# Optimization experiments

Measured on AMD Instinct MI355X. Metric: run time of the kernel, lower is better.

Reference implementation:

```python
import jax, jax.numpy as jnp
import numpy as np

N_NODES = 50000
N_EDGES = 640000
IN_C, HID_C, OUT_C = 64, 128, 64


def _glorot(key, fan_in, fan_out):
    lim = float(np.sqrt(6.0 / (fan_in + fan_out)))
    return jax.random.uniform(key, (fan_in, fan_out), jnp.float32, -lim, lim)


def setup_inputs() -> dict:
    key = jax.random.key(0)
    ks = jax.random.split(key, 16)
    x = jax.random.normal(ks[0], (N_NODES, IN_C), jnp.float32)
    edge_index = jax.random.randint(ks[1], (2, N_EDGES), 0, N_NODES, jnp.int64)
    # SAGEConv params: out = mean_aggr(x_j) @ Wl + x @ Wr + b
    dims = [(IN_C, HID_C), (HID_C, HID_C), (HID_C, OUT_C)]
    params = {}
    for i, (fi, fo) in enumerate(dims):
        params[f"Wl{i}"] = _glorot(ks[2 + 3 * i], fi, fo)
        params[f"Wr{i}"] = _glorot(ks[3 + 3 * i], fi, fo)
        params[f"b{i}"] = jnp.zeros((fo,), jnp.float32)
    # classifier: Linear(64,32) -> ReLU -> Linear(32,1) -> Sigmoid (dropout off in eval)
    params["Wc1"] = _glorot(ks[11], OUT_C, 32)
    params["bc1"] = jnp.zeros((32,), jnp.float32)
    params["Wc2"] = _glorot(ks[12], 32, 1)
    params["bc2"] = jnp.zeros((1,), jnp.float32)
    return {"x": x, "edge_index": edge_index, **params}


def _sage_conv(x, src, dst, Wl, Wr, b):
    # gather neighbor (source) features along edges, mean-aggregate at target
    msgs = x[src]                                                    # [E, C]
    agg = jax.ops.segment_sum(msgs, dst, num_segments=N_NODES)      # [N, C]
    deg = jax.ops.segment_sum(jnp.ones((src.shape[0], 1), x.dtype), dst,
                              num_segments=N_NODES)                 # [N, 1]
    agg = agg / jnp.maximum(deg, 1.0)
    return agg @ Wl + x @ Wr + b


def reference(x, edge_index, Wl0, Wr0, b0, Wl1, Wr1, b1, Wl2, Wr2, b2,
              Wc1, bc1, Wc2, bc2):
    src, dst = edge_index[0], edge_index[1]
    h = jax.nn.relu(_sage_conv(x, src, dst, Wl0, Wr0, b0))
    h = jax.nn.relu(_sage_conv(h, src, dst, Wl1, Wr1, b1))
    h = _sage_conv(h, src, dst, Wl2, Wr2, b2)                       # [N, 64]
    h = jax.nn.relu(h @ Wc1 + bc1)                                  # [N, 32]
    return jax.nn.sigmoid(h @ Wc2 + bc2)                            # [N, 1]
```

## Files before the change

kernel.cpp:

```cpp
#include <hip/hip_runtime.h>
#include <hip/hip_cooperative_groups.h>
#include <math.h>

namespace cg = cooperative_groups;

#define NN 50000
#define NE 640000
#define CAP 64

typedef short short8 __attribute__((ext_vector_type(8)));
typedef float f32x4  __attribute__((ext_vector_type(4)));

__device__ __forceinline__ unsigned bfr(float f) {
    unsigned u = __float_as_uint(f);
    return (u + 0x7FFFu + ((u >> 16) & 1u)) >> 16;
}
__device__ __forceinline__ unsigned pk2(float a, float b) { return bfr(a) | (bfr(b) << 16); }
__device__ __forceinline__ float bflo(unsigned u) { return __uint_as_float(u << 16); }
__device__ __forceinline__ float bfhi(unsigned u) { return __uint_as_float(u & 0xFFFF0000u); }

__device__ __forceinline__ void packOne(const float* Wl, const float* Wr,
                                        unsigned short* wp, int idx,
                                        int CIN, int COUT) {
    int k = idx / COUT, n = idx % COUT;
    float v = (k < CIN) ? Wl[k * COUT + n] : Wr[(k - CIN) * COUT + n];
    int kt = k >> 5, quad = (k >> 3) & 3, j = k & 7;
    int nt = n >> 4, l16 = n & 15;
    int NT = COUT / 16;
    wp[(((kt * NT + nt) * 64) + quad * 16 + l16) * 8 + j] = (unsigned short)bfr(v);
}

template <int LOGC>
__device__ __forceinline__ void
agg_phase(const unsigned* __restrict__ xu, const int* __restrict__ nbr,
          const int* __restrict__ cnt, unsigned* __restrict__ aggu,
          int wgl, int nwave, int lane) {
    constexpr int RU = 1 << (LOGC - 1);
    constexpr int PC = RU / 16;
    const int qw = lane >> 4, l16 = lane & 15;

    for (int gw = wgl; gw < NN; gw += nwave) {
        const int deg = cnt[gw];
        const int m = (deg < CAP) ? deg : CAP;

        int idx = 0;
        if (lane < m) idx = nbr[gw * CAP + lane];

        float a[2 * PC] = {};

#pragma unroll 4
        for (int j = 0; j < m; j += 4) {
            const int n = __shfl(idx, (j + qw) & 63);
            const bool valid = (j + qw) < m;
            if (PC == 2) {
                const uint2 u = *(const uint2*)(xu + (size_t)n * RU + l16 * 2);
                if (valid) {
                    a[0] += bflo(u.x); a[1] += bfhi(u.x);
                    a[2] += bflo(u.y); a[3] += bfhi(u.y);
                }
            } else {
                const uint4 u = *(const uint4*)(xu + (size_t)n * RU + l16 * 4);
                if (valid) {
                    a[0] += bflo(u.x); a[1] += bfhi(u.x);
                    a[2] += bflo(u.y); a[3] += bfhi(u.y);
                    a[4] += bflo(u.z); a[5] += bfhi(u.z);
                    a[6] += bflo(u.w); a[7] += bfhi(u.w);
                }
            }
        }

#pragma unroll
        for (int c = 0; c < 2 * PC; ++c) {
            a[c] += __shfl_xor(a[c], 16);
            a[c] += __shfl_xor(a[c], 32);
        }

        if (qw == 0) {
            const float di = 1.0f / (float)((deg > 1) ? deg : 1);
            if (PC == 2) {
                uint2 o = make_uint2(pk2(a[0] * di, a[1] * di), pk2(a[2] * di, a[3] * di));
                *(uint2*)(aggu + (size_t)gw * RU + l16 * 2) = o;
            } else {
                uint4 o = make_uint4(pk2(a[0] * di, a[1] * di), pk2(a[2] * di, a[3] * di),
                                     pk2(a[4] * di, a[5] * di), pk2(a[6] * di, a[7] * di));
                *(uint4*)(aggu + (size_t)gw * RU + l16 * 4) = o;
            }
        }
    }
}

template <int CIN, int COUT, bool RELU>
__device__ __forceinline__ void
mfma_phase(const unsigned short* __restrict__ Agg, const unsigned short* __restrict__ X,
           const unsigned short* __restrict__ Wpack, const float* __restrict__ bias,
           unsigned short* __restrict__ outp, int blk, int gstride, int wave, int lane) {
    constexpr int KT = (2 * CIN) / 32;
    constexpr int NT = COUT / 16;
    const int quad = lane >> 4, l16 = lane & 15;
    const int NTILE = (NN + 127) / 128;

    for (int tile = blk; tile < NTILE; tile += gstride) {
        const int row_base = tile * 128 + wave * 32;
        int r0 = row_base + l16;      if (r0 >= NN) r0 = NN - 1;
        int r1 = row_base + 16 + l16; if (r1 >= NN) r1 = NN - 1;

        f32x4 acc[2][NT] = {};

        for (int kt = 0; kt < KT; ++kt) {
            const unsigned short* P = (kt < KT / 2) ? Agg : X;
            const int kb = (kt < KT / 2) ? kt * 32 : kt * 32 - CIN;
            const short8 a0 = *(const short8*)(P + (size_t)r0 * CIN + kb + quad * 8);
            const short8 a1 = *(const short8*)(P + (size_t)r1 * CIN + kb + quad * 8);
#pragma unroll
            for (int nt = 0; nt < NT; ++nt) {
                const short8 bfrag = *(const short8*)(Wpack + (size_t)((kt * NT + nt) * 64 + lane) * 8);
                acc[0][nt] = __builtin_amdgcn_mfma_f32_16x16x32_bf16(a0, bfrag, acc[0][nt], 0, 0, 0);
                acc[1][nt] = __builtin_amdgcn_mfma_f32_16x16x32_bf16(a1, bfrag, acc[1][nt], 0, 0, 0);
            }
        }

#pragma unroll
        for (int nt = 0; nt < NT; ++nt) {
            const int col = nt * 16 + l16;
            const float bb = bias[col];
#pragma unroll
            for (int s = 0; s < 2; ++s) {
#pragma unroll
                for (int rg = 0; rg < 4; ++rg) {
                    int row = row_base + s * 16 + quad * 4 + rg;
                    if (row < NN) {
                        float v = acc[s][nt][rg] + bb;
                        if (RELU) v = fmaxf(v, 0.f);
                        outp[(size_t)row * COUT + col] = (unsigned short)bfr(v);
                    }
                }
            }
        }
    }
}

__global__ __launch_bounds__(256) void
k_all(const int* __restrict__ src, const int* __restrict__ dst,
      const float* __restrict__ x,
      const float* Wl0, const float* Wr0, const float* b0,
      const float* Wl1, const float* Wr1, const float* b1,
      const float* Wl2, const float* Wr2, const float* b2,
      const float* Wc1, const float* bc1, const float* Wc2, const float* bc2,
      int* cnt, int* nbr, unsigned short* xb,
      unsigned short* wp0, unsigned short* wp1, unsigned short* wp2,
      unsigned short* wpc,
      unsigned short* aggb, unsigned short* h0b, unsigned short* h1b,
      float* out) {
    cg::grid_group grid = cg::this_grid();

    __shared__ __align__(16) short Hs[8 * 16 * 64];

    const int t = threadIdx.x, b = blockIdx.x;
    const int nthr = gridDim.x * 256;
    const int nwave = nthr >> 6;
    const int gt = b * 256 + t;
    const int wave = t >> 6, lane = t & 63;
    const int wgl = gt >> 6;
    const int quad = lane >> 4, l16 = lane & 15;

    for (int e = gt; e < NE; e += nthr) {
        int d = dst[e];
        int p = atomicAdd(&cnt[d], 1);
        if (p < CAP) nbr[d * CAP + p] = src[e];
    }
    for (int i = gt; i < NN * 16; i += nthr) {
        float4 v = ((const float4*)x)[i];
        ((uint2*)xb)[i] = make_uint2(pk2(v.x, v.y), pk2(v.z, v.w));
    }
    for (int i = gt; i < 67584; i += nthr) {
        if (i < 16384) packOne(Wl0, Wr0, wp0, i, 64, 128);
        else if (i < 49152) packOne(Wl1, Wr1, wp1, i - 16384, 128, 128);
        else if (i < 65536) packOne(Wl2, Wr2, wp2, i - 49152, 128, 64);
        else packOne(Wc1, Wc1, wpc, i - 65536, 64, 32);
    }
    grid.sync();

    agg_phase<6>((const unsigned*)xb, nbr, cnt, (unsigned*)aggb, wgl, nwave, lane);
    grid.sync();
    mfma_phase<64, 128, true>(aggb, xb, wp0, b0, h0b, b, gridDim.x, wave, lane);
    grid.sync();

    agg_phase<7>((const unsigned*)h0b, nbr, cnt, (unsigned*)aggb, wgl, nwave, lane);
    grid.sync();
    mfma_phase<128, 128, true>(aggb, h0b, wp1, b1, h1b, b, gridDim.x, wave, lane);
    grid.sync();

    agg_phase<7>((const unsigned*)h1b, nbr, cnt, (unsigned*)aggb, wgl, nwave, lane);
    grid.sync();

    {
        constexpr int CIN = 128, NT = 4, KT = 8;
        const int NTILE = (NN + 127) / 128;

        for (int tile = b; tile < NTILE; tile += gridDim.x) {
            const int row_base = tile * 128 + wave * 32;
            int r0 = row_base + l16;      if (r0 >= NN) r0 = NN - 1;
            int r1 = row_base + 16 + l16; if (r1 >= NN) r1 = NN - 1;

            f32x4 acc[2][NT] = {};

            for (int kt = 0; kt < KT; ++kt) {
                const unsigned short* P = (kt < KT / 2) ? aggb : h1b;
                const int kb = (kt < KT / 2) ? kt * 32 : kt * 32 - CIN;
                const short8 a0 = *(const short8*)(P + (size_t)r0 * CIN + kb + quad * 8);
                const short8 a1 = *(const short8*)(P + (size_t)r1 * CIN + kb + quad * 8);
#pragma unroll
                for (int nt = 0; nt < NT; ++nt) {
                    const short8 bfrag = *(const short8*)(wp2 + (size_t)((kt * NT + nt) * 64 + lane) * 8);
                    acc[0][nt] = __builtin_amdgcn_mfma_f32_16x16x32_bf16(a0, bfrag, acc[0][nt], 0, 0, 0);
                    acc[1][nt] = __builtin_amdgcn_mfma_f32_16x16x32_bf16(a1, bfrag, acc[1][nt], 0, 0, 0);
                }
            }

#pragma unroll
            for (int nt = 0; nt < NT; ++nt) {
                const float bb = b2[nt * 16 + l16];
#pragma unroll
                for (int s = 0; s < 2; ++s)
#pragma unroll
                    for (int rg = 0; rg < 4; ++rg)
                        Hs[(wave * 2 + s) * 1024 + (quad * 4 + rg) * 64 + nt * 16 + l16] =
                            (unsigned short)bfr(acc[s][nt][rg] + bb);
            }
            __syncthreads();

            f32x4 sacc[2][2] = {};
#pragma unroll
            for (int s = 0; s < 2; ++s)
#pragma unroll
                for (int kt2 = 0; kt2 < 2; ++kt2) {
                    const short8 af = *(const short8*)&Hs[(wave * 2 + s) * 1024 + l16 * 64 +
                                                          kt2 * 32 + quad * 8];
#pragma unroll
                    for (int nt2 = 0; nt2 < 2; ++nt2) {
                        const short8 bf = *(const short8*)(wpc + (size_t)((kt2 * 2 + nt2) * 64 + lane) * 8);
                        sacc[s][nt2] = __builtin_amdgcn_mfma_f32_16x16x32_bf16(af, bf, sacc[s][nt2], 0, 0, 0);
                    }
                }

            const float b1a = bc1[l16], b1b = bc1[16 + l16];
            const float w2a = Wc2[l16], w2b = Wc2[16 + l16];
            const float b2v = bc2[0];
#pragma unroll
            for (int s = 0; s < 2; ++s)
#pragma unroll
                for (int rg = 0; rg < 4; ++rg) {
                    float p = fmaxf(sacc[s][0][rg] + b1a, 0.f) * w2a +
                              fmaxf(sacc[s][1][rg] + b1b, 0.f) * w2b;
#pragma unroll
                    for (int off = 1; off < 16; off <<= 1) p += __shfl_xor(p, off);
                    if (l16 == 0) {
                        int row = row_base + s * 16 + quad * 4 + rg;
                        if (row < NN) out[row] = 1.0f / (1.0f + expf(-(p + b2v)));
                    }
                }
            __syncthreads();
        }
    }
}

__global__ __launch_bounds__(256) void
k_prep(const int* __restrict__ src, const int* __restrict__ dst,
       int* __restrict__ cnt, int* __restrict__ nbr,
       const float* __restrict__ x, unsigned* __restrict__ xb,
       const float* Wl0, const float* Wr0, const float* Wl1, const float* Wr1,
       const float* Wl2, const float* Wr2, const float* Wc1,
       unsigned short* wp0, unsigned short* wp1, unsigned short* wp2,
       unsigned short* wpc) {
    const int b = blockIdx.x, t = threadIdx.x;
    if (b < 2500) {
        int e = b * 256 + t;
        if (e < NE) {
            int d = dst[e];
            int p = atomicAdd(&cnt[d], 1);
            if (p < CAP) nbr[d * CAP + p] = src[e];
        }
    } else if (b < 5625) {
        int i = (b - 2500) * 256 + t;
        if (i < NN * 16) {
            float4 v = ((const float4*)x)[i];
            ((uint2*)xb)[i] = make_uint2(pk2(v.x, v.y), pk2(v.z, v.w));
        }
    } else {
        int idx = (b - 5625) * 256 + t;
        if (idx < 16384) packOne(Wl0, Wr0, wp0, idx, 64, 128);
        else if (idx < 49152) packOne(Wl1, Wr1, wp1, idx - 16384, 128, 128);
        else if (idx < 65536) packOne(Wl2, Wr2, wp2, idx - 49152, 128, 64);
        else if (idx < 67584) packOne(Wc1, Wc1, wpc, idx - 65536, 64, 32);
    }
}

template <int LOGC>
__global__ __launch_bounds__(256) void
k_aggregate(const unsigned* __restrict__ xu, const int* __restrict__ nbr,
            const int* __restrict__ cnt, unsigned* __restrict__ aggu, int N) {
    const int wgl = (blockIdx.x * 256 + threadIdx.x) >> 6;
    if (wgl >= N) return;
    agg_phase<LOGC>(xu, nbr, cnt, aggu, wgl, 1 << 30, threadIdx.x & 63);
}

template <int CIN, int COUT, bool RELU>
__global__ __launch_bounds__(256) void
k_mfma(const unsigned short* __restrict__ Agg, const unsigned short* __restrict__ X,
       const unsigned short* __restrict__ Wpack, const float* __restrict__ bias,
       unsigned short* __restrict__ outp, int N) {
    mfma_phase<CIN, COUT, RELU>(Agg, X, Wpack, bias, outp,
                                blockIdx.x, 1 << 30, threadIdx.x >> 6, threadIdx.x & 63);
}

__global__ __launch_bounds__(256) void
k_mfma_cls(const unsigned short* __restrict__ Agg, const unsigned short* __restrict__ X,
           const unsigned short* __restrict__ Wpack, const unsigned short* __restrict__ WpackC,
           const float* __restrict__ bias, const float* __restrict__ bc1,
           const float* __restrict__ Wc2, const float* __restrict__ bc2,
           float* __restrict__ out, int N) {
    constexpr int CIN = 128, NT = 4, KT = 8;

    __shared__ __align__(16) short Hs[8 * 16 * 64];

    const int t = threadIdx.x;
    const int wave = t >> 6, lane = t & 63;
    const int quad = lane >> 4, l16 = lane & 15;

    const int row_base = blockIdx.x * 128 + wave * 32;
    int r0 = row_base + l16;      if (r0 >= N) r0 = N - 1;
    int r1 = row_base + 16 + l16; if (r1 >= N) r1 = N - 1;

    f32x4 acc[2][NT] = {};

    for (int kt = 0; kt < KT; ++kt) {
        const unsigned short* P = (kt < KT / 2) ? Agg : X;
        const int kb = (kt < KT / 2) ? kt * 32 : kt * 32 - CIN;
        const short8 a0 = *(const short8*)(P + (size_t)r0 * CIN + kb + quad * 8);
        const short8 a1 = *(const short8*)(P + (size_t)r1 * CIN + kb + quad * 8);
#pragma unroll
        for (int nt = 0; nt < NT; ++nt) {
            const short8 bfrag = *(const short8*)(Wpack + (size_t)((kt * NT + nt) * 64 + lane) * 8);
            acc[0][nt] = __builtin_amdgcn_mfma_f32_16x16x32_bf16(a0, bfrag, acc[0][nt], 0, 0, 0);
            acc[1][nt] = __builtin_amdgcn_mfma_f32_16x16x32_bf16(a1, bfrag, acc[1][nt], 0, 0, 0);
        }
    }

#pragma unroll
    for (int nt = 0; nt < NT; ++nt) {
        const float bb = bias[nt * 16 + l16];
#pragma unroll
        for (int s = 0; s < 2; ++s)
#pragma unroll
            for (int rg = 0; rg < 4; ++rg)
                Hs[(wave * 2 + s) * 1024 + (quad * 4 + rg) * 64 + nt * 16 + l16] =
                    (unsigned short)bfr(acc[s][nt][rg] + bb);
    }
    __syncthreads();

    f32x4 sacc[2][2] = {};
#pragma unroll
    for (int s = 0; s < 2; ++s)
#pragma unroll
        for (int kt2 = 0; kt2 < 2; ++kt2) {
            const short8 af = *(const short8*)&Hs[(wave * 2 + s) * 1024 + l16 * 64 +
                                                  kt2 * 32 + quad * 8];
#pragma unroll
            for (int nt2 = 0; nt2 < 2; ++nt2) {
                const short8 bf = *(const short8*)(WpackC + (size_t)((kt2 * 2 + nt2) * 64 + lane) * 8);
                sacc[s][nt2] = __builtin_amdgcn_mfma_f32_16x16x32_bf16(af, bf, sacc[s][nt2], 0, 0, 0);
            }
        }

    const float b1a = bc1[l16], b1b = bc1[16 + l16];
    const float w2a = Wc2[l16], w2b = Wc2[16 + l16];
    const float b2v = bc2[0];
#pragma unroll
    for (int s = 0; s < 2; ++s)
#pragma unroll
        for (int rg = 0; rg < 4; ++rg) {
            float p = fmaxf(sacc[s][0][rg] + b1a, 0.f) * w2a +
                      fmaxf(sacc[s][1][rg] + b1b, 0.f) * w2b;
#pragma unroll
            for (int off = 1; off < 16; off <<= 1) p += __shfl_xor(p, off);
            if (l16 == 0) {
                int row = row_base + s * 16 + quad * 4 + rg;
                if (row < N) out[row] = 1.0f / (1.0f + expf(-(p + b2v)));
            }
        }
}

extern "C" void kernel_launch(void* const* d_in, const int* in_sizes, int n_in,
                              void* d_out, int out_size, void* d_ws, size_t ws_size,
                              hipStream_t stream) {
    const float* x   = (const float*)d_in[0];
    const int*   ei  = (const int*)d_in[1];
    const int*   src = ei;
    const int*   dst = ei + NE;
    const float* Wl0 = (const float*)d_in[2];
    const float* Wr0 = (const float*)d_in[3];
    const float* b0  = (const float*)d_in[4];
    const float* Wl1 = (const float*)d_in[5];
    const float* Wr1 = (const float*)d_in[6];
    const float* b1  = (const float*)d_in[7];
    const float* Wl2 = (const float*)d_in[8];
    const float* Wr2 = (const float*)d_in[9];
    const float* b2  = (const float*)d_in[10];
    const float* Wc1 = (const float*)d_in[11];
    const float* bc1 = (const float*)d_in[12];
    const float* Wc2 = (const float*)d_in[13];
    const float* bc2 = (const float*)d_in[14];
    float* out = (float*)d_out;

    char*  ws   = (char*)d_ws;
    int*   cnt  = (int*)(ws);
    unsigned short* wp0 = (unsigned short*)(ws + (size_t)256 * 1024);
    unsigned short* wp1 = (unsigned short*)(ws + (size_t)352 * 1024);
    unsigned short* wp2 = (unsigned short*)(ws + (size_t)448 * 1024);
    unsigned short* wpc = (unsigned short*)(ws + (size_t)512 * 1024);
    int*   nbr  = (int*)(ws + (size_t)1 * (1 << 20));
    unsigned short* xb   = (unsigned short*)(ws + (size_t)16 * (1 << 20));
    unsigned short* aggb = (unsigned short*)(ws + (size_t)24 * (1 << 20));
    unsigned short* h0b  = (unsigned short*)(ws + (size_t)40 * (1 << 20));
    unsigned short* h1b  = (unsigned short*)(ws + (size_t)56 * (1 << 20));

    hipMemsetAsync(cnt, 0, (size_t)NN * sizeof(int), stream);

    bool coop_ok = false;
    int maxBpc = 0, ncu = 0, dev = 0;
    hipGetDevice(&dev);
    hipDeviceGetAttribute(&ncu, hipDeviceAttributeMultiprocessorCount, dev);
    hipError_t qerr = hipOccupancyMaxActiveBlocksPerMultiprocessor(
        &maxBpc, (const void*)k_all, 256, 0);
    if (qerr == hipSuccess && maxBpc > 0 && ncu > 0) {
        int grid = maxBpc * ncu;
        if (grid > 2048) grid = 2048;
        const int* srcp = src; const int* dstp = dst;
        void* args[] = {
            (void*)&srcp, (void*)&dstp, (void*)&x,
            (void*)&Wl0, (void*)&Wr0, (void*)&b0,
            (void*)&Wl1, (void*)&Wr1, (void*)&b1,
            (void*)&Wl2, (void*)&Wr2, (void*)&b2,
            (void*)&Wc1, (void*)&bc1, (void*)&Wc2, (void*)&bc2,
            (void*)&cnt, (void*)&nbr, (void*)&xb,
            (void*)&wp0, (void*)&wp1, (void*)&wp2, (void*)&wpc,
            (void*)&aggb, (void*)&h0b, (void*)&h1b,
            (void*)&out
        };
        hipError_t lerr = hipLaunchCooperativeKernel((const void*)k_all, dim3(grid),
                                                     dim3(256), args, 0, stream);
        if (lerr == hipSuccess) coop_ok = true;
        else (void)hipGetLastError();
    } else {
        (void)hipGetLastError();
    }

    if (!coop_ok) {
        const int B = 256;
        const int AGG_GRID = (NN + 3) / 4;
        const int MFMA_GRID = (NN + 127) / 128;

        k_prep<<<5889, B, 0, stream>>>(src, dst, cnt, nbr, x, (unsigned*)xb,
                                       Wl0, Wr0, Wl1, Wr1, Wl2, Wr2, Wc1,
                                       wp0, wp1, wp2, wpc);

        k_aggregate<6><<<AGG_GRID, B, 0, stream>>>((const unsigned*)xb, nbr, cnt,
                                                   (unsigned*)aggb, NN);
        k_mfma<64, 128, true><<<MFMA_GRID, B, 0, stream>>>(aggb, xb, wp0, b0, h0b, NN);

        k_aggregate<7><<<AGG_GRID, B, 0, stream>>>((const unsigned*)h0b, nbr, cnt,
                                                   (unsigned*)aggb, NN);
        k_mfma<128, 128, true><<<MFMA_GRID, B, 0, stream>>>(aggb, h0b, wp1, b1, h1b, NN);

        k_aggregate<7><<<AGG_GRID, B, 0, stream>>>((const unsigned*)h1b, nbr, cnt,
                                                   (unsigned*)aggb, NN);
        k_mfma_cls<<<MFMA_GRID, B, 0, stream>>>(aggb, h1b, wp2, wpc, b2, bc1, Wc2, bc2,
                                                out, NN);
    }
}
```

Before: 231.9 us.

## Halve MFMA row tiles per wave and raise occupancy bound for cooperative kernel

```diff
diff --git a/kernel.cpp b/kernel.cpp
--- a/kernel.cpp
+++ b/kernel.cpp
@@ -97,25 +97,22 @@
     constexpr int KT = (2 * CIN) / 32;
     constexpr int NT = COUT / 16;
     const int quad = lane >> 4, l16 = lane & 15;
-    const int NTILE = (NN + 127) / 128;
+    const int NTILE = (NN + 63) / 64;
 
     for (int tile = blk; tile < NTILE; tile += gstride) {
-        const int row_base = tile * 128 + wave * 32;
-        int r0 = row_base + l16;      if (r0 >= NN) r0 = NN - 1;
-        int r1 = row_base + 16 + l16; if (r1 >= NN) r1 = NN - 1;
-
-        f32x4 acc[2][NT] = {};
+        const int row_base = tile * 64 + wave * 16;
+        int r0 = row_base + l16; if (r0 >= NN) r0 = NN - 1;
+
+        f32x4 acc[NT] = {};
 
         for (int kt = 0; kt < KT; ++kt) {
             const unsigned short* P = (kt < KT / 2) ? Agg : X;
             const int kb = (kt < KT / 2) ? kt * 32 : kt * 32 - CIN;
             const short8 a0 = *(const short8*)(P + (size_t)r0 * CIN + kb + quad * 8);
-            const short8 a1 = *(const short8*)(P + (size_t)r1 * CIN + kb + quad * 8);
 #pragma unroll
             for (int nt = 0; nt < NT; ++nt) {
                 const short8 bfrag = *(const short8*)(Wpack + (size_t)((kt * NT + nt) * 64 + lane) * 8);
-                acc[0][nt] = __builtin_amdgcn_mfma_f32_16x16x32_bf16(a0, bfrag, acc[0][nt], 0, 0, 0);
-                acc[1][nt] = __builtin_amdgcn_mfma_f32_16x16x32_bf16(a1, bfrag, acc[1][nt], 0, 0, 0);
+                acc[nt] = __builtin_amdgcn_mfma_f32_16x16x32_bf16(a0, bfrag, acc[nt], 0, 0, 0);
             }
         }
 
@@ -124,22 +121,87 @@
             const int col = nt * 16 + l16;
             const float bb = bias[col];
 #pragma unroll
-            for (int s = 0; s < 2; ++s) {
-#pragma unroll
-                for (int rg = 0; rg < 4; ++rg) {
-                    int row = row_base + s * 16 + quad * 4 + rg;
-                    if (row < NN) {
-                        float v = acc[s][nt][rg] + bb;
-                        if (RELU) v = fmaxf(v, 0.f);
-                        outp[(size_t)row * COUT + col] = (unsigned short)bfr(v);
-                    }
+            for (int rg = 0; rg < 4; ++rg) {
+                int row = row_base + quad * 4 + rg;
+                if (row < NN) {
+                    float v = acc[nt][rg] + bb;
+                    if (RELU) v = fmaxf(v, 0.f);
+                    outp[(size_t)row * COUT + col] = (unsigned short)bfr(v);
                 }
             }
         }
     }
 }
 
-__global__ __launch_bounds__(256) void
+__device__ __forceinline__ void
+cls_phase(const unsigned short* __restrict__ Agg, const unsigned short* __restrict__ X,
+          const unsigned short* __restrict__ Wpack, const unsigned short* __restrict__ WpackC,
+          const float* __restrict__ bias, const float* __restrict__ bc1,
+          const float* __restrict__ Wc2, const float* __restrict__ bc2,
+          float* __restrict__ out, short* __restrict__ Hs,
+          int blk, int gstride, int wave, int lane) {
+    constexpr int CIN = 128, NT = 4, KT = 8;
+    const int quad = lane >> 4, l16 = lane & 15;
+    const int NTILE = (NN + 63) / 64;
+
+    for (int tile = blk; tile < NTILE; tile += gstride) {
+        const int row_base = tile * 64 + wave * 16;
+        int r0 = row_base + l16; if (r0 >= NN) r0 = NN - 1;
+
+        f32x4 acc[NT] = {};
+
+        for (int kt = 0; kt < KT; ++kt) {
+            const unsigned short* P = (kt < KT / 2) ? Agg : X;
+            const int kb = (kt < KT / 2) ? kt * 32 : kt * 32 - CIN;
+            const short8 a0 = *(const short8*)(P + (size_t)r0 * CIN + kb + quad * 8);
+#pragma unroll
+            for (int nt = 0; nt < NT; ++nt) {
+                const short8 bfrag = *(const short8*)(Wpack + (size_t)((kt * NT + nt) * 64 + lane) * 8);
+                acc[nt] = __builtin_amdgcn_mfma_f32_16x16x32_bf16(a0, bfrag, acc[nt], 0, 0, 0);
+            }
+        }
+
+        short* hw = Hs + wave * 1024;
+#pragma unroll
+        for (int nt = 0; nt < NT; ++nt) {
+            const float bb = bias[nt * 16 + l16];
+#pragma unroll
+            for (int rg = 0; rg < 4; ++rg)
+                hw[(quad * 4 + rg) * 64 + nt * 16 + l16] =
+                    (unsigned short)bfr(acc[nt][rg] + bb);
+        }
+        __syncthreads();
+
+        f32x4 sacc[2] = {};
+#pragma unroll
+        for (int kt2 = 0; kt2 < 2; ++kt2) {
+            const short8 af = *(const short8*)&hw[l16 * 64 + kt2 * 32 + quad * 8];
+#pragma unroll
+            for (int nt2 = 0; nt2 < 2; ++nt2) {
+                const short8 bf = *(const short8*)(WpackC + (size_t)((kt2 * 2 + nt2) * 64 + lane) * 8);
+                sacc[nt2] = __builtin_amdgcn_mfma_f32_16x16x32_bf16(af, bf, sacc[nt2], 0, 0, 0);
+            }
+        }
+
+        const float b1a = bc1[l16], b1b = bc1[16 + l16];
+        const float w2a = Wc2[l16], w2b = Wc2[16 + l16];
+        const float b2v = bc2[0];
+#pragma unroll
+        for (int rg = 0; rg < 4; ++rg) {
+            float p = fmaxf(sacc[0][rg] + b1a, 0.f) * w2a +
+                      fmaxf(sacc[1][rg] + b1b, 0.f) * w2b;
+#pragma unroll
+            for (int off = 1; off < 16; off <<= 1) p += __shfl_xor(p, off);
+            if (l16 == 0) {
+                int row = row_base + quad * 4 + rg;
+                if (row < NN) out[row] = 1.0f / (1.0f + expf(-(p + b2v)));
+            }
+        }
+        __syncthreads();
+    }
+}
+
+__global__ __launch_bounds__(256, 4) void
 k_all(const int* __restrict__ src, const int* __restrict__ dst,
       const float* __restrict__ x,
       const float* Wl0, const float* Wr0, const float* b0,
@@ -153,7 +215,7 @@
       float* out) {
     cg::grid_group grid = cg::this_grid();
 
-    __shared__ __align__(16) short Hs[8 * 16 * 64];
+    __shared__ __align__(16) short Hs[4 * 16 * 64];
 
     const int t = threadIdx.x, b = blockIdx.x;
     const int nthr = gridDim.x * 256;
@@ -161,7 +223,6 @@
     const int gt = b * 256 + t;
     const int wave = t >> 6, lane = t & 63;
     const int wgl = gt >> 6;
-    const int quad = lane >> 4, l16 = lane & 15;
 
     for (int e = gt; e < NE; e += nthr) {
         int d = dst[e];
@@ -192,76 +253,7 @@
 
     agg_phase<7>((const unsigned*)h1b, nbr, cnt, (unsigned*)aggb, wgl, nwave, lane);
     grid.sync();
-
-    {
-        constexpr int CIN = 128, NT = 4, KT = 8;
-        const int NTILE = (NN + 127) / 128;
-
-        for (int tile = b; tile < NTILE; tile += gridDim.x) {
-            const int row_base = tile * 128 + wave * 32;
-            int r0 = row_base + l16;      if (r0 >= NN) r0 = NN - 1;
-            int r1 = row_base + 16 + l16; if (r1 >= NN) r1 = NN - 1;
-
-            f32x4 acc[2][NT] = {};
-
-            for (int kt = 0; kt < KT; ++kt) {
-                const unsigned short* P = (kt < KT / 2) ? aggb : h1b;
-                const int kb = (kt < KT / 2) ? kt * 32 : kt * 32 - CIN;
-                const short8 a0 = *(const short8*)(P + (size_t)r0 * CIN + kb + quad * 8);
-                const short8 a1 = *(const short8*)(P + (size_t)r1 * CIN + kb + quad * 8);
-#pragma unroll
-                for (int nt = 0; nt < NT; ++nt) {
-                    const short8 bfrag = *(const short8*)(wp2 + (size_t)((kt * NT + nt) * 64 + lane) * 8);
-                    acc[0][nt] = __builtin_amdgcn_mfma_f32_16x16x32_bf16(a0, bfrag, acc[0][nt], 0, 0, 0);
-                    acc[1][nt] = __builtin_amdgcn_mfma_f32_16x16x32_bf16(a1, bfrag, acc[1][nt], 0, 0, 0);
-                }
-            }
-
-#pragma unroll
-            for (int nt = 0; nt < NT; ++nt) {
-                const float bb = b2[nt * 16 + l16];
-#pragma unroll
-                for (int s = 0; s < 2; ++s)
-#pragma unroll
-                    for (int rg = 0; rg < 4; ++rg)
-                        Hs[(wave * 2 + s) * 1024 + (quad * 4 + rg) * 64 + nt * 16 + l16] =
-                            (unsigned short)bfr(acc[s][nt][rg] + bb);
-            }
-            __syncthreads();
-
-            f32x4 sacc[2][2] = {};
-#pragma unroll
-            for (int s = 0; s < 2; ++s)
-#pragma unroll
-                for (int kt2 = 0; kt2 < 2; ++kt2) {
-                    const short8 af = *(const short8*)&Hs[(wave * 2 + s) * 1024 + l16 * 64 +
-                                                          kt2 * 32 + quad * 8];
-#pragma unroll
-                    for (int nt2 = 0; nt2 < 2; ++nt2) {
-                        const short8 bf = *(const short8*)(wpc + (size_t)((kt2 * 2 + nt2) * 64 + lane) * 8);
-                        sacc[s][nt2] = __builtin_amdgcn_mfma_f32_16x16x32_bf16(af, bf, sacc[s][nt2], 0, 0, 0);
-                    }
-                }
-
-            const float b1a = bc1[l16], b1b = bc1[16 + l16];
-            const float w2a = Wc2[l16], w2b = Wc2[16 + l16];
-            const float b2v = bc2[0];
-#pragma unroll
-            for (int s = 0; s < 2; ++s)
-#pragma unroll
-                for (int rg = 0; rg < 4; ++rg) {
-                    float p = fmaxf(sacc[s][0][rg] + b1a, 0.f) * w2a +
-                              fmaxf(sacc[s][1][rg] + b1b, 0.f) * w2b;
-#pragma unroll
-                    for (int off = 1; off < 16; off <<= 1) p += __shfl_xor(p, off);
-                    if (l16 == 0) {
-                        int row = row_base + s * 16 + quad * 4 + rg;
-                        if (row < NN) out[row] = 1.0f / (1.0f + expf(-(p + b2v)));
-                    }
-                }
-            __syncthreads();
-        }
-    }
+    cls_phase(aggb, h1b, wp2, wpc, b2, bc1, Wc2, bc2, out, Hs, b, gridDim.x, wave, lane);
 }
 
 __global__ __launch_bounds__(256) void
@@ -319,75 +311,9 @@
            const float* __restrict__ bias, const float* __restrict__ bc1,
            const float* __restrict__ Wc2, const float* __restrict__ bc2,
            float* __restrict__ out, int N) {
-    constexpr int CIN = 128, NT = 4, KT = 8;
-
-    __shared__ __align__(16) short Hs[8 * 16 * 64];
-
-    const int t = threadIdx.x;
-    const int wave = t >> 6, lane = t & 63;
-    const int quad = lane >> 4, l16 = lane & 15;
-
-    const int row_base = blockIdx.x * 128 + wave * 32;
-    int r0 = row_base + l16;      if (r0 >= N) r0 = N - 1;
-    int r1 = row_base + 16 + l16; if (r1 >= N) r1 = N - 1;
-
-    f32x4 acc[2][NT] = {};
-
-    for (int kt = 0; kt < KT; ++kt) {
-        const unsigned short* P = (kt < KT / 2) ? Agg : X;
-        const int kb = (kt < KT / 2) ? kt * 32 : kt * 32 - CIN;
-        const short8 a0 = *(const short8*)(P + (size_t)r0 * CIN + kb + quad * 8);
-        const short8 a1 = *(const short8*)(P + (size_t)r1 * CIN + kb + quad * 8);
-#pragma unroll
-        for (int nt = 0; nt < NT; ++nt) {
-            const short8 bfrag = *(const short8*)(Wpack + (size_t)((kt * NT + nt) * 64 + lane) * 8);
-            acc[0][nt] = __builtin_amdgcn_mfma_f32_16x16x32_bf16(a0, bfrag, acc[0][nt], 0, 0, 0);
-            acc[1][nt] = __builtin_amdgcn_mfma_f32_16x16x32_bf16(a1, bfrag, acc[1][nt], 0, 0, 0);
-        }
-    }
-
-#pragma unroll
-    for (int nt = 0; nt < NT; ++nt) {
-        const float bb = bias[nt * 16 + l16];
-#pragma unroll
-        for (int s = 0; s < 2; ++s)
-#pragma unroll
-            for (int rg = 0; rg < 4; ++rg)
-                Hs[(wave * 2 + s) * 1024 + (quad * 4 + rg) * 64 + nt * 16 + l16] =
-                    (unsigned short)bfr(acc[s][nt][rg] + bb);
-    }
-    __syncthreads();
-
-    f32x4 sacc[2][2] = {};
-#pragma unroll
-    for (int s = 0; s < 2; ++s)
-#pragma unroll
-        for (int kt2 = 0; kt2 < 2; ++kt2) {
-            const short8 af = *(const short8*)&Hs[(wave * 2 + s) * 1024 + l16 * 64 +
-                                                  kt2 * 32 + quad * 8];
-#pragma unroll
-            for (int nt2 = 0; nt2 < 2; ++nt2) {
-                const short8 bf = *(const short8*)(WpackC + (size_t)((kt2 * 2 + nt2) * 64 + lane) * 8);
-                sacc[s][nt2] = __builtin_amdgcn_mfma_f32_16x16x32_bf16(af, bf, sacc[s][nt2], 0, 0, 0);
-            }
-        }
-
-    const float b1a = bc1[l16], b1b = bc1[16 + l16];
-    const float w2a = Wc2[l16], w2b = Wc2[16 + l16];
-    const float b2v = bc2[0];
-#pragma unroll
-    for (int s = 0; s < 2; ++s)
-#pragma unroll
-        for (int rg = 0; rg < 4; ++rg) {
-            float p = fmaxf(sacc[s][0][rg] + b1a, 0.f) * w2a +
-                      fmaxf(sacc[s][1][rg] + b1b, 0.f) * w2b;
-#pragma unroll
-            for (int off = 1; off < 16; off <<= 1) p += __shfl_xor(p, off);
-            if (l16 == 0) {
-                int row = row_base + s * 16 + quad * 4 + rg;
-                if (row < N) out[row] = 1.0f / (1.0f + expf(-(p + b2v)));
-            }
-        }
+    __shared__ __align__(16) short Hs[4 * 16 * 64];
+    cls_phase(Agg, X, Wpack, WpackC, bias, bc1, Wc2, bc2, out, Hs,
+              blockIdx.x, 1 << 30, threadIdx.x >> 6, threadIdx.x & 63);
 }
 
 extern "C" void kernel_launch(void* const* d_in, const int* in_sizes, int n_in,
@@ -458,7 +384,7 @@
     if (!coop_ok) {
         const int B = 256;
         const int AGG_GRID = (NN + 3) / 4;
-        const int MFMA_GRID = (NN + 127) / 128;
+        const int MFMA_GRID = (NN + 63) / 64;
 
         k_prep<<<5889, B, 0, stream>>>(src, dst, cnt, nbr, x, (unsigned*)xb,
                                        Wl0, Wr0, Wl1, Wr1, Wl2, Wr2, Wc1,
```

Result: slower. 780.9 us (+236.7%).
